# Performance work log

Measured on AMD Instinct MI355X. Metric: run time of the kernel, lower is better.

## Reference

```python
import jax, jax.numpy as jnp
import numpy as np

N_NODES = 100000
D_IN = 128
D_OUT = 128
SHAPES = {"r1": 1, "r2": 2, "r3": 3}
N_EDGES = {"r1": 400000, "r2": 300000, "r3": 200000}


def setup_inputs() -> dict:
    key = jax.random.key(0)
    ks = jax.random.split(key, 10)
    inp = {
        "x": jax.random.normal(ks[0], (N_NODES, D_IN), dtype=jnp.float32),
        "A_r1": jax.random.normal(ks[1], (D_IN * 1, D_OUT), dtype=jnp.float32) * 0.05,
        "A_r2": jax.random.normal(ks[2], (D_IN * 2, D_OUT), dtype=jnp.float32) * 0.05,
        "A_r3": jax.random.normal(ks[3], (D_IN * 3, D_OUT), dtype=jnp.float32) * 0.05,
        "C_w": jax.random.normal(ks[4], (D_IN, D_OUT), dtype=jnp.float32) * 0.05,
        "C_b": jax.random.normal(ks[5], (D_OUT,), dtype=jnp.float32) * 0.05,
    }
    for j, (name, shape) in enumerate(SHAPES.items()):
        n = N_EDGES[name] * shape
        inp[f"ei_{name}"] = jax.random.randint(ks[6 + j], (2, n), 0, N_NODES, dtype=jnp.int64)
    return inp


def _edge_type_agg(x, edge_indices, A, shape):
    # edge_indices: [2, n_edges*shape]; row0 = sources, row1 reshaped -> dest per hyperedge
    dest = edge_indices[1].reshape(-1, shape)[:, 0]          # [n_edges]
    gathered = x[edge_indices[0]].reshape(-1, shape * x.shape[1])  # [n_edges, shape*D_IN]
    msg = gathered @ A                                        # [n_edges, D_OUT]
    # 1/count(dest) normalization (torch.unique counts == per-type in-degree)
    deg = jax.ops.segment_sum(jnp.ones_like(dest, dtype=msg.dtype), dest, num_segments=x.shape[0])
    msg = msg / deg[dest][:, None]
    return jax.ops.segment_sum(msg, dest, num_segments=x.shape[0])  # scatter_add


def reference(x, ei_r1, ei_r2, ei_r3, A_r1, A_r2, A_r3, C_w, C_b):
    agg = (_edge_type_agg(x, ei_r1, A_r1, 1)
           + _edge_type_agg(x, ei_r2, A_r2, 2)
           + _edge_type_agg(x, ei_r3, A_r3, 3))
    return x @ C_w + C_b + agg
```

## Files before the change

kernel.cpp:

```cpp
#include <hip/hip_runtime.h>

#define N_NODES 100000
#define D 128

typedef unsigned short u16;
typedef short s16x8 __attribute__((ext_vector_type(8)));
typedef float f32x4 __attribute__((ext_vector_type(4)));


#define ENTS_OFF 2804224L
#define AT_OFF   9204224L
#define XB_OFF   9433600L

__device__ __forceinline__ u16 f2b(float f) {
    union { float f; unsigned u; } v; v.f = f;
    unsigned r = (v.u + 0x7FFFu + ((v.u >> 16) & 1u)) >> 16;
    return (u16)r;
}
__device__ __forceinline__ unsigned pk(float lo, float hi) {
    return (unsigned)f2b(lo) | ((unsigned)f2b(hi) << 16);
}
__device__ __forceinline__ float blo(unsigned w) { return __uint_as_float(w << 16); }
__device__ __forceinline__ float bhi(unsigned w) { return __uint_as_float(w & 0xFFFF0000u); }


__global__ __launch_bounds__(256) void init_kernel(
    const float* __restrict__ x,
    const float* __restrict__ A1, const float* __restrict__ A2,
    const float* __restrict__ A3, const float* __restrict__ Cw,
    u16* __restrict__ ATb, u16* __restrict__ xb, int* __restrict__ deg) {
    int b = blockIdx.x, t = threadIdx.x;
    if (b < 293) {
        int i0 = (b * 256 + t) * 4;
#pragma unroll
        for (int r = 0; r < 4; r++)
            if (i0 + r < 300000) deg[i0 + r] = 0;
        return;
    }
    if (b < 741) {
        int mb = b - 293;
        int m = mb >> 6;
        int idx = (mb & 63) * 256 + t;
        int n = idx >> 7, kk = idx & 127;
        const float* src; int srow;
        if (m == 0)      { src = A1; srow = kk; }
        else if (m < 3)  { src = A2; srow = (m - 1) * 128 + kk; }
        else if (m < 6)  { src = A3; srow = (m - 3) * 128 + kk; }
        else             { src = Cw; srow = kk; }
        ATb[m * 16384 + n * 128 + kk] = f2b(src[(long)srow * 128 + n]);
        return;
    }
    int f = (b - 741) * 256 + t;
    int node = f >> 4, j = f & 15;
    const float* xr = x + (long)node * 128 + j * 8;
    float4 v0 = *(const float4*)xr;
    float4 v1 = *(const float4*)(xr + 4);
    uint4 o;
    o.x = pk(v0.x, v0.y); o.y = pk(v0.z, v0.w);
    o.z = pk(v1.x, v1.y); o.w = pk(v1.z, v1.w);
    *(uint4*)(xb + (long)node * 128 + j * 8) = o;
}


__global__ __launch_bounds__(256) void deg_all(
    const int* __restrict__ e1, const int* __restrict__ e2, const int* __restrict__ e3,
    int ne1, int ne2, int ne3, int* __restrict__ deg) {
    int g = blockIdx.x * 256 + threadIdx.x;
    if (g < ne1) {
        atomicAdd(&deg[e1[ne1 + g]], 1);
    } else if (g < ne1 + ne2) {
        int e = g - ne1;
        atomicAdd(&deg[N_NODES + e2[ne2 * 2 + e * 2]], 1);
    } else if (g < ne1 + ne2 + ne3) {
        int e = g - ne1 - ne2;
        atomicAdd(&deg[2 * N_NODES + e3[ne3 * 3 + e * 3]], 1);
    }
}

__device__ __forceinline__ int ucnt(const int* deg, int d) {
    return deg[d] + 2 * deg[N_NODES + d] + 3 * deg[2 * N_NODES + d];
}


__global__ __launch_bounds__(256) void scan_reduce_u(const int* __restrict__ deg,
                                                     int* __restrict__ bsums, int n) {
    __shared__ int s[256];
    int t = threadIdx.x;
    int base = blockIdx.x * 1024 + t * 4;
    int loc = 0;
#pragma unroll
    for (int r = 0; r < 4; r++) {
        int idx = base + r;
        if (idx < n) loc += ucnt(deg, idx);
    }
    s[t] = loc;
    for (int off = 128; off > 0; off >>= 1) {
        __syncthreads();
        if (t < off) s[t] += s[t + off];
    }
    if (t == 0) bsums[blockIdx.x] = s[0];
}

__global__ __launch_bounds__(512) void scan_tops(const int* __restrict__ bsums,
                                                 int* __restrict__ boffs,
                                                 int* __restrict__ offs, int nb, int n) {
    __shared__ int s[512];
    int t = threadIdx.x;
    int v = (t < nb) ? bsums[t] : 0;
    s[t] = v;
    for (int off = 1; off < 512; off <<= 1) {
        __syncthreads();
        int x = (t >= off) ? s[t - off] : 0;
        __syncthreads();
        s[t] += x;
    }
    if (t < nb) boffs[t] = s[t] - v;
    if (t == nb - 1) offs[n] = s[t];
}

__global__ __launch_bounds__(256) void scan_final_u(
    const int* __restrict__ deg, const int* __restrict__ boffs,
    int* __restrict__ offs, int* __restrict__ cursor, int n) {
    __shared__ int s[256];
    int t = threadIdx.x;
    int base = blockIdx.x * 1024 + t * 4;
    int v[4], p[4];
#pragma unroll
    for (int r = 0; r < 4; r++) {
        int idx = base + r;
        v[r] = (idx < n) ? ucnt(deg, idx) : 0;
    }
    p[0] = 0; p[1] = v[0]; p[2] = v[0] + v[1]; p[3] = v[0] + v[1] + v[2];
    int tsum = p[3] + v[3];
    s[t] = tsum;
    for (int off = 1; off < 256; off <<= 1) {
        __syncthreads();
        int x = (t >= off) ? s[t - off] : 0;
        __syncthreads();
        s[t] += x;
    }
    int texcl = s[t] - tsum + boffs[blockIdx.x];
#pragma unroll
    for (int r = 0; r < 4; r++) {
        int idx = base + r;
        if (idx < n) {
            int val = texcl + p[r];
            offs[idx] = val;
            int c1 = deg[idx], c2 = deg[N_NODES + idx];
            cursor[idx] = val;
            cursor[N_NODES + idx] = val + c1;
            cursor[2 * N_NODES + idx] = val + c1 + 2 * c2;
        }
    }
}


__global__ __launch_bounds__(256) void scatter_all(
    const int* __restrict__ e1, const int* __restrict__ e2, const int* __restrict__ e3,
    int ne1, int ne2, int ne3, const int* __restrict__ deg,
    int* __restrict__ cursor, int* __restrict__ ents) {
    int g = blockIdx.x * 256 + threadIdx.x;
    if (g < ne1) {
        int dest = e1[ne1 + g];
        int pos = atomicAdd(&cursor[dest], 1);
        ents[pos] = e1[g];
    } else if (g < ne1 + ne2) {
        int e = g - ne1;
        int dest = e2[ne2 * 2 + e * 2];
        int c2 = deg[N_NODES + dest];
        int pos = atomicAdd(&cursor[N_NODES + dest], 1);
        ents[pos]      = e2[e * 2];
        ents[pos + c2] = e2[e * 2 + 1];
    } else if (g < ne1 + ne2 + ne3) {
        int e = g - ne1 - ne2;
        int dest = e3[ne3 * 3 + e * 3];
        int c3 = deg[2 * N_NODES + dest];
        int pos = atomicAdd(&cursor[2 * N_NODES + dest], 1);
        ents[pos]          = e3[e * 3];
        ents[pos + c3]     = e3[e * 3 + 1];
        ents[pos + 2 * c3] = e3[e * 3 + 2];
    }
}


__global__ __launch_bounds__(256) void agg_gemm(
    const u16* __restrict__ xb, const int* __restrict__ ents,
    const int* __restrict__ offs, const int* __restrict__ deg,
    const u16* __restrict__ AT, const float* __restrict__ Cb,
    float* __restrict__ out) {
    __shared__ __align__(16) u16 Xs[4][64][40];
    __shared__ int4 meta[64];

    const int t = threadIdx.x;
    const int d0 = blockIdx.x * 64;
    const int lane = t & 63, wv = t >> 6;
    const int nbase = wv * 32, quad = lane >> 4, lrow = lane & 15;
    const int col = lane * 2;

    if (t < 64) {
        int dd = (d0 + t < N_NODES) ? d0 + t : N_NODES - 1;
        meta[t] = make_int4(offs[dd], deg[dd], deg[N_NODES + dd], deg[2 * N_NODES + dd]);
    }
    __syncthreads();

    f32x4 acc[4][2];
#pragma unroll
    for (int mi = 0; mi < 4; mi++)
#pragma unroll
        for (int ni = 0; ni < 2; ni++) acc[mi][ni] = (f32x4)(0.0f);

#pragma unroll
    for (int s = 0; s < 7; s++) {
        if (s < 6) {
            for (int j = 0; j < 16; j++) {
                int row = wv * 16 + j;
                int4 m = meta[row];
                int cnt = (s == 0) ? m.y : (s < 3) ? m.z : m.w;
                int base = m.x + (s >= 1 ? m.y : 0) + (s >= 2 ? m.z : 0) +
                           (s >= 3 ? m.z : 0) + (s >= 4 ? m.w : 0) + (s >= 5 ? m.w : 0);
                float al = 0.0f, ah = 0.0f;
                for (int p = 0; p < cnt; p += 4) {
                    unsigned w[4];
#pragma unroll
                    for (int i = 0; i < 4; i++) {
                        int q = (p + i < cnt) ? p + i : cnt - 1;
                        int src = ents[base + q];
                        unsigned v = *(const unsigned*)(xb + (long)src * 128 + col);
                        w[i] = (p + i < cnt) ? v : 0u;
                    }
#pragma unroll
                    for (int i = 0; i < 4; i++) { al += blo(w[i]); ah += bhi(w[i]); }
                }
                float inv = cnt ? 1.0f / (float)cnt : 0.0f;
                *(unsigned*)&Xs[col >> 5][row][col & 31] = pk(al * inv, ah * inv);
            }
        } else {
#pragma unroll
            for (int i = 0; i < 4; i++) {
                int f = i * 256 + t;
                int row = f >> 4, k8 = f & 15;
                long rs = (d0 + row < N_NODES) ? d0 + row : N_NODES - 1;
                uint4 v = *(const uint4*)(xb + rs * 128 + k8 * 8);
                *(uint4*)&Xs[k8 >> 2][row][(k8 & 3) * 8] = v;
            }
        }
        __syncthreads();
        const u16* B = AT + s * 16384;
#pragma unroll
        for (int c = 0; c < 4; c++) {
            s16x8 a[4], b2[2];
#pragma unroll
            for (int mi = 0; mi < 4; mi++)
                a[mi] = *(const s16x8*)&Xs[c][mi * 16 + lrow][quad * 8];
#pragma unroll
            for (int ni = 0; ni < 2; ni++)
                b2[ni] = *(const s16x8*)(B + (nbase + ni * 16 + lrow) * 128 +
                                         c * 32 + quad * 8);
#pragma unroll
            for (int mi = 0; mi < 4; mi++)
#pragma unroll
                for (int ni = 0; ni < 2; ni++)
                    acc[mi][ni] = __builtin_amdgcn_mfma_f32_16x16x32_bf16(
                        a[mi], b2[ni], acc[mi][ni], 0, 0, 0);
        }
        __syncthreads();
    }

    float* smf = (float*)&Xs[0][0][0];
#pragma unroll
    for (int h = 0; h < 2; h++) {
        if (h) __syncthreads();
#pragma unroll
        for (int mi = 2 * h; mi < 2 * h + 2; mi++)
#pragma unroll
            for (int ni = 0; ni < 2; ni++)
#pragma unroll
                for (int reg = 0; reg < 4; reg++) {
                    int row = (mi - 2 * h) * 16 + quad * 4 + reg;
                    int cq = nbase + ni * 16 + lrow;
                    smf[row * 132 + cq] = acc[mi][ni][reg];
                }
        __syncthreads();
#pragma unroll
        for (int i = 0; i < 4; i++) {
            int f = i * 256 + t;
            int row = f >> 5, cq = (f & 31) * 4;
            int gr = d0 + h * 32 + row;
            if (gr < N_NODES) {
                float4 v = *(const float4*)&smf[row * 132 + cq];
                float4 b = *(const float4*)&Cb[cq];
                v.x += b.x; v.y += b.y; v.z += b.z; v.w += b.w;
                *(float4*)&out[(long)gr * 128 + cq] = v;
            }
        }
    }
}


extern "C" void kernel_launch(void* const* d_in, const int* in_sizes, int n_in,
                              void* d_out, int out_size, void* d_ws, size_t ws_size,
                              hipStream_t stream) {
    const float* x  = (const float*)d_in[0];
    const float* A1 = (const float*)d_in[1];
    const float* A2 = (const float*)d_in[2];
    const float* A3 = (const float*)d_in[3];
    const float* Cw = (const float*)d_in[4];
    const float* Cb = (const float*)d_in[5];
    const int* e1 = (const int*)d_in[6];
    const int* e2 = (const int*)d_in[7];
    const int* e3 = (const int*)d_in[8];
    float* out = (float*)d_out;

    int* ws = (int*)d_ws;
    int* deg    = ws;
    int* offs   = ws + 300000;
    int* cursor = ws + 400001;
    int* bsums  = ws + 700001;
    int* boffs  = ws + 700513;
    int* ents   = (int*)((char*)d_ws + ENTS_OFF);
    u16* ATb    = (u16*)((char*)d_ws + AT_OFF);
    u16* xb     = (u16*)((char*)d_ws + XB_OFF);

    const int NE1 = in_sizes[6] / 2;
    const int NE2 = in_sizes[7] / (2 * 2);
    const int NE3 = in_sizes[8] / (2 * 3);
    const int NET = NE1 + NE2 + NE3;
    const int n = N_NODES;
    const int NB = (n + 1023) / 1024;

    init_kernel<<<293 + 448 + 6250, 256, 0, stream>>>(x, A1, A2, A3, Cw, ATb, xb, deg);
    deg_all<<<(NET + 255) / 256, 256, 0, stream>>>(e1, e2, e3, NE1, NE2, NE3, deg);
    scan_reduce_u<<<NB, 256, 0, stream>>>(deg, bsums, n);
    scan_tops<<<1, 512, 0, stream>>>(bsums, boffs, offs, NB, n);
    scan_final_u<<<NB, 256, 0, stream>>>(deg, boffs, offs, cursor, n);
    scatter_all<<<(NET + 255) / 256, 256, 0, stream>>>(e1, e2, e3, NE1, NE2, NE3,
                                                       deg, cursor, ents);
    agg_gemm<<<(N_NODES + 63) / 64, 256, 0, stream>>>(xb, ents, offs, deg, ATb, Cb, out);
}
```

Measured before the change: 435.0 us.

## Merge degree counting into init, use decoupled lookback scan, restructure aggregation GEMM

Folds the degree atomics into the bf16 conversion kernel and moves zeroing into its own small kernel. The three-pass prefix scan becomes a single decoupled-lookback pass, so fewer kernels are launched. The aggregation kernel now uses 32-node tiles with 512 threads and gathers all six neighbor slots in one pass with more loads in flight. The six MFMA slots then run back to back from a larger shared-memory buffer instead of alternating gather and GEMM. The lookback spins on flags set by earlier blocks and assumes those blocks are already running.

```diff
diff --git a/kernel.cpp b/kernel.cpp
--- a/kernel.cpp
+++ b/kernel.cpp
@@ -24,23 +24,31 @@
 __device__ __forceinline__ float bhi(unsigned w) { return __uint_as_float(w & 0xFFFF0000u); }
 
 
-__global__ __launch_bounds__(256) void init_kernel(
+__global__ __launch_bounds__(256) void zero_kernel(int* __restrict__ deg,
+                                                   int* __restrict__ flags) {
+    int b = blockIdx.x, t = threadIdx.x;
+    if (b < 293) {
+        int i0 = (b * 256 + t) * 4;
+#pragma unroll
+        for (int r = 0; r < 4; r++)
+            if (i0 + r < 300000) deg[i0 + r] = 0;
+    } else {
+        if (t < 128) flags[t] = 0;
+    }
+}
+
+
+__global__ __launch_bounds__(256) void init_deg(
     const float* __restrict__ x,
     const float* __restrict__ A1, const float* __restrict__ A2,
     const float* __restrict__ A3, const float* __restrict__ Cw,
+    const int* __restrict__ e1, const int* __restrict__ e2, const int* __restrict__ e3,
+    int ne1, int ne2, int ne3,
     u16* __restrict__ ATb, u16* __restrict__ xb, int* __restrict__ deg) {
     int b = blockIdx.x, t = threadIdx.x;
-    if (b < 293) {
-        int i0 = (b * 256 + t) * 4;
-#pragma unroll
-        for (int r = 0; r < 4; r++)
-            if (i0 + r < 300000) deg[i0 + r] = 0;
-        return;
-    }
-    if (b < 741) {
-        int mb = b - 293;
-        int m = mb >> 6;
-        int idx = (mb & 63) * 256 + t;
+    if (b < 448) {
+        int m = b >> 6;
+        int idx = (b & 63) * 256 + t;
         int n = idx >> 7, kk = idx & 127;
         const float* src; int srow;
         if (m == 0)      { src = A1; srow = kk; }
@@ -50,22 +58,19 @@
         ATb[m * 16384 + n * 128 + kk] = f2b(src[(long)srow * 128 + n]);
         return;
     }
-    int f = (b - 741) * 256 + t;
-    int node = f >> 4, j = f & 15;
-    const float* xr = x + (long)node * 128 + j * 8;
-    float4 v0 = *(const float4*)xr;
-    float4 v1 = *(const float4*)(xr + 4);
-    uint4 o;
-    o.x = pk(v0.x, v0.y); o.y = pk(v0.z, v0.w);
-    o.z = pk(v1.x, v1.y); o.w = pk(v1.z, v1.w);
-    *(uint4*)(xb + (long)node * 128 + j * 8) = o;
-}
-
-
-__global__ __launch_bounds__(256) void deg_all(
-    const int* __restrict__ e1, const int* __restrict__ e2, const int* __restrict__ e3,
-    int ne1, int ne2, int ne3, int* __restrict__ deg) {
-    int g = blockIdx.x * 256 + threadIdx.x;
+    if (b < 6698) {
+        int f = (b - 448) * 256 + t;
+        int node = f >> 4, j = f & 15;
+        const float* xr = x + (long)node * 128 + j * 8;
+        float4 v0 = *(const float4*)xr;
+        float4 v1 = *(const float4*)(xr + 4);
+        uint4 o;
+        o.x = pk(v0.x, v0.y); o.y = pk(v0.z, v0.w);
+        o.z = pk(v1.x, v1.y); o.w = pk(v1.z, v1.w);
+        *(uint4*)(xb + (long)node * 128 + j * 8) = o;
+        return;
+    }
+    int g = (b - 6698) * 256 + t;
     if (g < ne1) {
         atomicAdd(&deg[e1[ne1 + g]], 1);
     } else if (g < ne1 + ne2) {
@@ -77,58 +82,24 @@
     }
 }
 
-__device__ __forceinline__ int ucnt(const int* deg, int d) {
-    return deg[d] + 2 * deg[N_NODES + d] + 3 * deg[2 * N_NODES + d];
-}
-
-
-__global__ __launch_bounds__(256) void scan_reduce_u(const int* __restrict__ deg,
-                                                     int* __restrict__ bsums, int n) {
+
+__global__ __launch_bounds__(256) void scan_lookback(
+    const int* __restrict__ deg, int* __restrict__ offs, int* __restrict__ cursor,
+    int* __restrict__ flags, int n, int nb) {
     __shared__ int s[256];
-    int t = threadIdx.x;
-    int base = blockIdx.x * 1024 + t * 4;
-    int loc = 0;
+    __shared__ int bprefix;
+    int t = threadIdx.x, bid = blockIdx.x;
+    int base = bid * 1024 + t * 4;
+    int d1[4], d2[4], v[4], p[4];
 #pragma unroll
     for (int r = 0; r < 4; r++) {
         int idx = base + r;
-        if (idx < n) loc += ucnt(deg, idx);
-    }
-    s[t] = loc;
-    for (int off = 128; off > 0; off >>= 1) {
-        __syncthreads();
-        if (t < off) s[t] += s[t + off];
-    }
-    if (t == 0) bsums[blockIdx.x] = s[0];
-}
-
-__global__ __launch_bounds__(512) void scan_tops(const int* __restrict__ bsums,
-                                                 int* __restrict__ boffs,
-                                                 int* __restrict__ offs, int nb, int n) {
-    __shared__ int s[512];
-    int t = threadIdx.x;
-    int v = (t < nb) ? bsums[t] : 0;
-    s[t] = v;
-    for (int off = 1; off < 512; off <<= 1) {
-        __syncthreads();
-        int x = (t >= off) ? s[t - off] : 0;
-        __syncthreads();
-        s[t] += x;
-    }
-    if (t < nb) boffs[t] = s[t] - v;
-    if (t == nb - 1) offs[n] = s[t];
-}
-
-__global__ __launch_bounds__(256) void scan_final_u(
-    const int* __restrict__ deg, const int* __restrict__ boffs,
-    int* __restrict__ offs, int* __restrict__ cursor, int n) {
-    __shared__ int s[256];
-    int t = threadIdx.x;
-    int base = blockIdx.x * 1024 + t * 4;
-    int v[4], p[4];
-#pragma unroll
-    for (int r = 0; r < 4; r++) {
-        int idx = base + r;
-        v[r] = (idx < n) ? ucnt(deg, idx) : 0;
+        if (idx < n) {
+            d1[r] = deg[idx];
+            d2[r] = deg[N_NODES + idx];
+            int d3 = deg[2 * N_NODES + idx];
+            v[r] = d1[r] + 2 * d2[r] + 3 * d3;
+        } else { d1[r] = 0; d2[r] = 0; v[r] = 0; }
     }
     p[0] = 0; p[1] = v[0]; p[2] = v[0] + v[1]; p[3] = v[0] + v[1] + v[2];
     int tsum = p[3] + v[3];
@@ -139,17 +110,39 @@
         __syncthreads();
         s[t] += x;
     }
-    int texcl = s[t] - tsum + boffs[blockIdx.x];
+    __syncthreads();
+    int total = s[255];
+    if (t == 0) {
+        int run = 0;
+        if (bid == 0) {
+            atomicExch(&flags[0], (total << 2) | 2);
+        } else {
+            atomicExch(&flags[bid], (total << 2) | 1);
+            int j = bid - 1;
+            while (true) {
+                int f = atomicAdd(&flags[j], 0);
+                int st = f & 3;
+                if (st == 0) continue;
+                run += (f >> 2);
+                if (st == 2) break;
+                j--;
+            }
+            atomicExch(&flags[bid], ((run + total) << 2) | 2);
+        }
+        bprefix = run;
+        if (bid == nb - 1) offs[n] = run + total;
+    }
+    __syncthreads();
+    int texcl = s[t] - tsum + bprefix;
 #pragma unroll
     for (int r = 0; r < 4; r++) {
         int idx = base + r;
         if (idx < n) {
             int val = texcl + p[r];
             offs[idx] = val;
-            int c1 = deg[idx], c2 = deg[N_NODES + idx];
             cursor[idx] = val;
-            cursor[N_NODES + idx] = val + c1;
-            cursor[2 * N_NODES + idx] = val + c1 + 2 * c2;
+            cursor[N_NODES + idx] = val + d1[r];
+            cursor[2 * N_NODES + idx] = val + d1[r] + 2 * d2[r];
         }
     }
 }
@@ -183,115 +176,150 @@
 }
 
 
-__global__ __launch_bounds__(256) void agg_gemm(
+__global__ __launch_bounds__(512) void agg_gemm(
     const u16* __restrict__ xb, const int* __restrict__ ents,
     const int* __restrict__ offs, const int* __restrict__ deg,
     const u16* __restrict__ AT, const float* __restrict__ Cb,
     float* __restrict__ out) {
-    __shared__ __align__(16) u16 Xs[4][64][40];
-    __shared__ int4 meta[64];
+    __shared__ __align__(16) u16 T[6 * 5120];
+    __shared__ int4 meta[32];
 
     const int t = threadIdx.x;
-    const int d0 = blockIdx.x * 64;
+    const int d0 = blockIdx.x * 32;
     const int lane = t & 63, wv = t >> 6;
-    const int nbase = wv * 32, quad = lane >> 4, lrow = lane & 15;
     const int col = lane * 2;
-
-    if (t < 64) {
+    const u16* xcol = xb + col;
+    const int ch = lane >> 4;
+    const int cw = col & 31;
+
+    if (t < 32) {
         int dd = (d0 + t < N_NODES) ? d0 + t : N_NODES - 1;
         meta[t] = make_int4(offs[dd], deg[dd], deg[N_NODES + dd], deg[2 * N_NODES + dd]);
     }
     __syncthreads();
 
-    f32x4 acc[4][2];
-#pragma unroll
-    for (int mi = 0; mi < 4; mi++)
-#pragma unroll
-        for (int ni = 0; ni < 2; ni++) acc[mi][ni] = (f32x4)(0.0f);
-
-#pragma unroll
-    for (int s = 0; s < 7; s++) {
-        if (s < 6) {
-            for (int j = 0; j < 16; j++) {
-                int row = wv * 16 + j;
-                int4 m = meta[row];
-                int cnt = (s == 0) ? m.y : (s < 3) ? m.z : m.w;
-                int base = m.x + (s >= 1 ? m.y : 0) + (s >= 2 ? m.z : 0) +
-                           (s >= 3 ? m.z : 0) + (s >= 4 ? m.w : 0) + (s >= 5 ? m.w : 0);
-                float al = 0.0f, ah = 0.0f;
-                for (int p = 0; p < cnt; p += 4) {
-                    unsigned w[4];
-#pragma unroll
-                    for (int i = 0; i < 4; i++) {
-                        int q = (p + i < cnt) ? p + i : cnt - 1;
-                        int src = ents[base + q];
-                        unsigned v = *(const unsigned*)(xb + (long)src * 128 + col);
-                        w[i] = (p + i < cnt) ? v : 0u;
-                    }
-#pragma unroll
-                    for (int i = 0; i < 4; i++) { al += blo(w[i]); ah += bhi(w[i]); }
-                }
-                float inv = cnt ? 1.0f / (float)cnt : 0.0f;
-                *(unsigned*)&Xs[col >> 5][row][col & 31] = pk(al * inv, ah * inv);
-            }
-        } else {
-#pragma unroll
-            for (int i = 0; i < 4; i++) {
-                int f = i * 256 + t;
-                int row = f >> 4, k8 = f & 15;
-                long rs = (d0 + row < N_NODES) ? d0 + row : N_NODES - 1;
-                uint4 v = *(const uint4*)(xb + rs * 128 + k8 * 8);
-                *(uint4*)&Xs[k8 >> 2][row][(k8 & 3) * 8] = v;
-            }
-        }
-        __syncthreads();
-        const u16* B = AT + s * 16384;
+    for (int j = 0; j < 4; j++) {
+        const int row = wv * 4 + j;
+        const int4 mm = meta[row];
+        const int lo = mm.x, c1 = mm.y, c2 = mm.z, c3 = mm.w;
+        float a0l = 0, a0h = 0, a1l = 0, a1h = 0, a2l = 0, a2h = 0;
+        float a3l = 0, a3h = 0, a4l = 0, a4h = 0, a5l = 0, a5h = 0;
+
+        for (int p = 0; p < c1; p += 4) {
+            unsigned w[4];
+#pragma unroll
+            for (int i = 0; i < 4; i++) {
+                int q = (p + i < c1) ? p + i : c1 - 1;
+                unsigned v = *(const unsigned*)(xcol + ((size_t)(unsigned)ents[lo + q] << 7));
+                w[i] = (p + i < c1) ? v : 0u;
+            }
+#pragma unroll
+            for (int i = 0; i < 4; i++) { a0l += blo(w[i]); a0h += bhi(w[i]); }
+        }
+        const int o1 = lo + c1;
+        for (int p = 0; p < c2; p += 4) {
+            unsigned wa[4], wb[4];
+#pragma unroll
+            for (int i = 0; i < 4; i++) {
+                int q = (p + i < c2) ? p + i : c2 - 1;
+                unsigned va = *(const unsigned*)(xcol + ((size_t)(unsigned)ents[o1 + q] << 7));
+                unsigned vb = *(const unsigned*)(xcol + ((size_t)(unsigned)ents[o1 + q + c2] << 7));
+                bool ok = p + i < c2;
+                wa[i] = ok ? va : 0u; wb[i] = ok ? vb : 0u;
+            }
+#pragma unroll
+            for (int i = 0; i < 4; i++) {
+                a1l += blo(wa[i]); a1h += bhi(wa[i]);
+                a2l += blo(wb[i]); a2h += bhi(wb[i]);
+            }
+        }
+        const int o3 = o1 + 2 * c2;
+        for (int p = 0; p < c3; p += 4) {
+            unsigned wa[4], wb[4], wc[4];
+#pragma unroll
+            for (int i = 0; i < 4; i++) {
+                int q = (p + i < c3) ? p + i : c3 - 1;
+                unsigned va = *(const unsigned*)(xcol + ((size_t)(unsigned)ents[o3 + q] << 7));
+                unsigned vb = *(const unsigned*)(xcol + ((size_t)(unsigned)ents[o3 + q + c3] << 7));
+                unsigned vc = *(const unsigned*)(xcol + ((size_t)(unsigned)ents[o3 + q + 2 * c3] << 7));
+                bool ok = p + i < c3;
+                wa[i] = ok ? va : 0u; wb[i] = ok ? vb : 0u; wc[i] = ok ? vc : 0u;
+            }
+#pragma unroll
+            for (int i = 0; i < 4; i++) {
+                a3l += blo(wa[i]); a3h += bhi(wa[i]);
+                a4l += blo(wb[i]); a4h += bhi(wb[i]);
+                a5l += blo(wc[i]); a5h += bhi(wc[i]);
+            }
+        }
+        const float i1 = c1 ? 1.0f / (float)c1 : 0.0f;
+        const float i2 = c2 ? 1.0f / (float)c2 : 0.0f;
+        const float i3 = c3 ? 1.0f / (float)c3 : 0.0f;
+        *(unsigned*)&T[((0 * 4 + ch) * 32 + row) * 40 + cw] = pk(a0l * i1, a0h * i1);
+        *(unsigned*)&T[((1 * 4 + ch) * 32 + row) * 40 + cw] = pk(a1l * i2, a1h * i2);
+        *(unsigned*)&T[((2 * 4 + ch) * 32 + row) * 40 + cw] = pk(a2l * i2, a2h * i2);
+        *(unsigned*)&T[((3 * 4 + ch) * 32 + row) * 40 + cw] = pk(a3l * i3, a3h * i3);
+        *(unsigned*)&T[((4 * 4 + ch) * 32 + row) * 40 + cw] = pk(a4l * i3, a4h * i3);
+        *(unsigned*)&T[((5 * 4 + ch) * 32 + row) * 40 + cw] = pk(a5l * i3, a5h * i3);
+    }
+    __syncthreads();
+
+    const int nbase = wv * 16, quad = lane >> 4, lrow = lane & 15;
+    f32x4 acc[2];
+    acc[0] = (f32x4)(0.0f); acc[1] = (f32x4)(0.0f);
+
+    auto mfma_slot = [&](int ts, int sw) {
+        const u16* B = AT + sw * 16384;
+        s16x8 bf[4];
+#pragma unroll
+        for (int c = 0; c < 4; c++)
+            bf[c] = *(const s16x8*)(B + (nbase + lrow) * 128 + c * 32 + quad * 8);
 #pragma unroll
         for (int c = 0; c < 4; c++) {
-            s16x8 a[4], b2[2];
-#pragma unroll
-            for (int mi = 0; mi < 4; mi++)
-                a[mi] = *(const s16x8*)&Xs[c][mi * 16 + lrow][quad * 8];
-#pragma unroll
-            for (int ni = 0; ni < 2; ni++)
-                b2[ni] = *(const s16x8*)(B + (nbase + ni * 16 + lrow) * 128 +
-                                         c * 32 + quad * 8);
-#pragma unroll
-            for (int mi = 0; mi < 4; mi++)
-#pragma unroll
-                for (int ni = 0; ni < 2; ni++)
-                    acc[mi][ni] = __builtin_amdgcn_mfma_f32_16x16x32_bf16(
-                        a[mi], b2[ni], acc[mi][ni], 0, 0, 0);
-        }
-        __syncthreads();
-    }
-
-    float* smf = (float*)&Xs[0][0][0];
-#pragma unroll
-    for (int h = 0; h < 2; h++) {
-        if (h) __syncthreads();
-#pragma unroll
-        for (int mi = 2 * h; mi < 2 * h + 2; mi++)
-#pragma unroll
-            for (int ni = 0; ni < 2; ni++)
-#pragma unroll
-                for (int reg = 0; reg < 4; reg++) {
-                    int row = (mi - 2 * h) * 16 + quad * 4 + reg;
-                    int cq = nbase + ni * 16 + lrow;
-                    smf[row * 132 + cq] = acc[mi][ni][reg];
-                }
-        __syncthreads();
-#pragma unroll
-        for (int i = 0; i < 4; i++) {
-            int f = i * 256 + t;
-            int row = f >> 5, cq = (f & 31) * 4;
-            int gr = d0 + h * 32 + row;
-            if (gr < N_NODES) {
-                float4 v = *(const float4*)&smf[row * 132 + cq];
-                float4 b = *(const float4*)&Cb[cq];
-                v.x += b.x; v.y += b.y; v.z += b.z; v.w += b.w;
-                *(float4*)&out[(long)gr * 128 + cq] = v;
-            }
+            s16x8 av0 = *(const s16x8*)&T[((ts * 4 + c) * 32 + lrow) * 40 + quad * 8];
+            s16x8 av1 = *(const s16x8*)&T[((ts * 4 + c) * 32 + 16 + lrow) * 40 + quad * 8];
+            acc[0] = __builtin_amdgcn_mfma_f32_16x16x32_bf16(av0, bf[c], acc[0], 0, 0, 0);
+            acc[1] = __builtin_amdgcn_mfma_f32_16x16x32_bf16(av1, bf[c], acc[1], 0, 0, 0);
+        }
+    };
+
+    mfma_slot(0, 0);
+    __syncthreads();
+
+    {
+        int row = t >> 4, k8 = t & 15;
+        long rs = (d0 + row < N_NODES) ? d0 + row : N_NODES - 1;
+        uint4 v = *(const uint4*)(xb + rs * 128 + k8 * 8);
+        *(uint4*)&T[((k8 >> 2) * 32 + row) * 40 + (k8 & 3) * 8] = v;
+    }
+    mfma_slot(1, 1);
+    mfma_slot(2, 2);
+    mfma_slot(3, 3);
+    mfma_slot(4, 4);
+    mfma_slot(5, 5);
+    __syncthreads();
+    mfma_slot(0, 6);
+    __syncthreads();
+
+    float* smf = (float*)T;
+#pragma unroll
+    for (int m = 0; m < 2; m++)
+#pragma unroll
+        for (int reg = 0; reg < 4; reg++) {
+            int row = m * 16 + quad * 4 + reg;
+            smf[row * 132 + nbase + lrow] = acc[m][reg];
+        }
+    __syncthreads();
+#pragma unroll
+    for (int i = 0; i < 2; i++) {
+        int f = i * 512 + t;
+        int row = f >> 5, cq = (f & 31) * 4;
+        int gr = d0 + row;
+        if (gr < N_NODES) {
+            float4 v = *(const float4*)&smf[row * 132 + cq];
+            float4 b = *(const float4*)&Cb[cq];
+            v.x += b.x; v.y += b.y; v.z += b.z; v.w += b.w;
+            *(float4*)&out[(long)gr * 128 + cq] = v;
         }
     }
 }
@@ -315,8 +343,7 @@
     int* deg    = ws;
     int* offs   = ws + 300000;
     int* cursor = ws + 400001;
-    int* bsums  = ws + 700001;
-    int* boffs  = ws + 700513;
+    int* flags  = ws + 700001;
     int* ents   = (int*)((char*)d_ws + ENTS_OFF);
     u16* ATb    = (u16*)((char*)d_ws + AT_OFF);
     u16* xb     = (u16*)((char*)d_ws + XB_OFF);
@@ -328,12 +355,11 @@
     const int n = N_NODES;
     const int NB = (n + 1023) / 1024;
 
-    init_kernel<<<293 + 448 + 6250, 256, 0, stream>>>(x, A1, A2, A3, Cw, ATb, xb, deg);
-    deg_all<<<(NET + 255) / 256, 256, 0, stream>>>(e1, e2, e3, NE1, NE2, NE3, deg);
-    scan_reduce_u<<<NB, 256, 0, stream>>>(deg, bsums, n);
-    scan_tops<<<1, 512, 0, stream>>>(bsums, boffs, offs, NB, n);
-    scan_final_u<<<NB, 256, 0, stream>>>(deg, boffs, offs, cursor, n);
+    zero_kernel<<<294, 256, 0, stream>>>(deg, flags);
+    init_deg<<<448 + 6250 + (NET + 255) / 256, 256, 0, stream>>>(
+        x, A1, A2, A3, Cw, e1, e2, e3, NE1, NE2, NE3, ATb, xb, deg);
+    scan_lookback<<<NB, 256, 0, stream>>>(deg, offs, cursor, flags, n, NB);
     scatter_all<<<(NET + 255) / 256, 256, 0, stream>>>(e1, e2, e3, NE1, NE2, NE3,
                                                        deg, cursor, ents);
-    agg_gemm<<<(N_NODES + 63) / 64, 256, 0, stream>>>(xb, ents, offs, deg, ATb, Cb, out);
-}
+    agg_gemm<<<(N_NODES + 31) / 32, 512, 0, stream>>>(xb, ents, offs, deg, ATb, Cb, out);
+}
```

Result: slower. 498.4 us (+14.6%).
